# Performance work log

Hardware: AMD Instinct MI355X
Metric: run time of the kernel (lower is better)

The kernel has to match this reference:

```python
import jax, jax.numpy as jnp
import numpy as np

V, E, H, L, B = 32000, 128, 32, 64, 32


def setup_inputs() -> dict:
    key = jax.random.key(0)
    k0, k1, k2, k3, k4, k5 = jax.random.split(key, 6)
    stdv = 1.0 / np.sqrt(H)
    we = jax.random.uniform(k0, (V, E), minval=-stdv, maxval=stdv, dtype=jnp.float32)
    we = we.at[1].set(0.0)  # pad token row zeroed, as in original
    i2h1 = jax.random.uniform(k1, (E + H, H), minval=-stdv, maxval=stdv, dtype=jnp.float32)
    i2h2 = jax.random.uniform(k2, (E + H, H), minval=-stdv, maxval=stdv, dtype=jnp.float32)
    h2o = jax.random.uniform(k3, (2 * H, V), minval=-stdv, maxval=stdv, dtype=jnp.float32)
    bias = jnp.ones((1, H), dtype=jnp.float32)  # assigned after reset_parameters -> stays ones
    hidden_init = jax.random.normal(k4, (1, H), dtype=jnp.float32)  # plain buffer, not reset
    inp = jax.random.randint(k5, (L, B), 0, V, dtype=jnp.int64)
    return {"inp": inp, "we": we, "i2h1": i2h1, "i2h2": i2h2,
            "h2o": h2o, "bias": bias, "hidden_init": hidden_init}


def reference(inp, we, i2h1, i2h2, h2o, bias, hidden_init):
    Lr, Br = inp.shape
    Hh = hidden_init.shape[1]
    emb = we[inp]                                   # [L,B,E] embedding gather
    h0 = jnp.broadcast_to(hidden_init, (Br, Hh))    # [B,H]
    b = jnp.broadcast_to(bias, (Br, Hh))            # [B,H]

    def make_step(W):
        def step(h, e):
            h_new = jnp.tanh(jnp.concatenate([e, h], axis=1) @ W + b)
            return h_new, h_new
        return step

    # forward direction: hf[i] = hidden after consuming token i
    _, hf = jax.lax.scan(make_step(i2h1), h0, emb)
    # backward direction (scan over reversed time, flip back)
    _, hb_rev = jax.lax.scan(make_step(i2h2), h0, emb[::-1])
    hb = hb_rev[::-1]                               # hb[i] = bwd hidden after token i

    # original uses hiddenf[i] (pre-token-i fwd state) and hiddenb[i+1] (post-token-(i+1) bwd state)
    hf_used = jnp.concatenate([h0[None], hf[:-1]], axis=0)   # [L,B,H]
    hb_used = jnp.concatenate([hb[1:], h0[None]], axis=0)    # [L,B,H]

    hcat = jnp.concatenate([hf_used, hb_used], axis=-1)      # [L,B,2H]
    logits = jnp.einsum('lbh,hv->lbv', hcat, h2o)            # [L,B,V]
    return jax.nn.log_softmax(logits, axis=-1)
```

## Files before the change

### kernel.cpp

```cpp
#include <hip/hip_runtime.h>

#define V_SZ 32000
#define E_SZ 128
#define H_SZ 32
#define L_SZ 64
#define B_SZ 32
#define M_TOT 2048
#define K2 64
#define NVT 125
#define NMT 32

typedef __bf16 bf16x8 __attribute__((ext_vector_type(8)));
typedef float f32x4 __attribute__((ext_vector_type(4)));

__device__ __forceinline__ unsigned short f2bf(float f) {
    unsigned int u = __float_as_uint(f);
    u += 0x7FFFu + ((u >> 16) & 1u);
    return (unsigned short)(u >> 16);
}

__device__ __forceinline__ void load_bfrag(
    const __bf16* __restrict__ h2oT, int xcol, int wn, int lg, int lr,
    bf16x8 bfr[8][2]) {
    const int colbase = xcol * 256;
#pragma unroll
    for (int n = 0; n < 8; ++n) {
        int col = colbase + wn * 128 + n * 16 + lr;
        const __bf16* bp = h2oT + (size_t)col * K2 + lg * 8;
        bfr[n][0] = *(const bf16x8*)(bp);
        bfr[n][1] = *(const bf16x8*)(bp + 32);
    }
}

__device__ __forceinline__ void tile_gemm(
    const __bf16* __restrict__ hcat, int rowbase, int wm, int lg, int lr,
    const bf16x8 bfr[8][2], f32x4 acc[2][8]) {
    bf16x8 af[2][2];
#pragma unroll
    for (int m = 0; m < 2; ++m) {
        int row = rowbase + wm * 32 + m * 16 + lr;
#pragma unroll
        for (int kh = 0; kh < 2; ++kh)
            af[m][kh] = *(const bf16x8*)(hcat + row * K2 + kh * 32 + lg * 8);
    }
#pragma unroll
    for (int m = 0; m < 2; ++m)
#pragma unroll
        for (int n = 0; n < 8; ++n) acc[m][n] = (f32x4){0.f, 0.f, 0.f, 0.f};
#pragma unroll
    for (int n = 0; n < 8; ++n)
#pragma unroll
        for (int m = 0; m < 2; ++m) {
            acc[m][n] = __builtin_amdgcn_mfma_f32_16x16x32_bf16(af[m][0], bfr[n][0], acc[m][n], 0, 0, 0);
            acc[m][n] = __builtin_amdgcn_mfma_f32_16x16x32_bf16(af[m][1], bfr[n][1], acc[m][n], 0, 0, 0);
        }
}

__global__ __launch_bounds__(256) void k_prep_rnn(
    const int* __restrict__ inp, const float* __restrict__ we,
    const float* __restrict__ i2h1, const float* __restrict__ i2h2,
    const float* __restrict__ h2o, const float* __restrict__ bias,
    const float* __restrict__ hinit,
    unsigned short* __restrict__ hcat_u, unsigned short* __restrict__ h2oT_u) {
    const int tid = threadIdx.x;
    const int p = blockIdx.x;
    if (p < 125) {
        const int v = p * 256 + tid;
        unsigned int* dst = (unsigned int*)(h2oT_u + (size_t)v * K2);
#pragma unroll
        for (int k = 0; k < K2; k += 2) {
            float a = h2o[(size_t)k * V_SZ + v];
            float b = h2o[(size_t)(k + 1) * V_SZ + v];
            dst[k >> 1] = (unsigned int)f2bf(a) | ((unsigned int)f2bf(b) << 16);
        }
        return;
    }
    const int w2 = p - 125;
    const int dir = w2 >> 4;
    const int bpair = w2 & 15;
    const float* W = dir ? i2h2 : i2h1;
    __shared__ float Xl[L_SZ * 2 * H_SZ];
    {
        const int j = tid & 31, bb = (tid >> 5) & 1, to = tid >> 6;
        const int b = bpair * 2 + bb;
        const float bj = bias[j];
        for (int tt = 0; tt < 16; ++tt) {
            const int t = to * 16 + tt;
            const int idx = inp[t * B_SZ + b];
            const float* er = we + (size_t)idx * E_SZ;
            float acc = bj;
#pragma unroll
            for (int k0 = 0; k0 < E_SZ; k0 += 4) {
                f32x4 e4 = *(const f32x4*)(er + k0);
                acc += e4.x * W[(k0 + 0) * H_SZ + j];
                acc += e4.y * W[(k0 + 1) * H_SZ + j];
                acc += e4.z * W[(k0 + 2) * H_SZ + j];
                acc += e4.w * W[(k0 + 3) * H_SZ + j];
            }
            Xl[(t * 2 + bb) * H_SZ + j] = acc;
        }
    }
    __syncthreads();
    if (tid < 64) {
        const int lane = tid;
        const int bb = lane >> 5;
        const int b = bpair * 2 + bb;
        const int j = lane & 31;
        const int srcbase = lane & 32;
        float wh[H_SZ];
#pragma unroll
        for (int k = 0; k < H_SZ; ++k) wh[k] = W[(E_SZ + k) * H_SZ + j];
        float h = hinit[j];
        for (int step = 0; step < L_SZ; ++step) {
            const int tt = dir ? (L_SZ - 1 - step) : step;
            hcat_u[(tt * B_SZ + b) * K2 + dir * H_SZ + j] = f2bf(h);
            float a0 = Xl[(tt * 2 + bb) * H_SZ + j];
            float a1 = 0.f, a2 = 0.f, a3 = 0.f;
#pragma unroll
            for (int k = 0; k < H_SZ; k += 4) {
                a0 += __shfl(h, srcbase | k, 64) * wh[k];
                a1 += __shfl(h, srcbase | (k + 1), 64) * wh[k + 1];
                a2 += __shfl(h, srcbase | (k + 2), 64) * wh[k + 2];
                a3 += __shfl(h, srcbase | (k + 3), 64) * wh[k + 3];
            }
            float x2 = (a0 + a1) + (a2 + a3);
            float e = __expf(2.f * x2);
            h = 1.f - 2.f * __builtin_amdgcn_rcpf(e + 1.f);
        }
    }
}

__global__ __launch_bounds__(256) void k_pass_a(
    const __bf16* __restrict__ hcat, const __bf16* __restrict__ h2oT,
    float* __restrict__ Asum) {
    const int tid = threadIdx.x;
    const int wave = tid >> 6, lane = tid & 63;
    const int wm = wave >> 1, wn = wave & 1;
    const int lg = lane >> 4, lr = lane & 15;
    const int rowbase = blockIdx.y * 64;
    bf16x8 bfr[8][2];
    load_bfrag(h2oT, blockIdx.x, wn, lg, lr, bfr);
    f32x4 acc[2][8];
    tile_gemm(hcat, rowbase, wm, lg, lr, bfr, acc);
    float rs[2][4];
#pragma unroll
    for (int m = 0; m < 2; ++m)
#pragma unroll
        for (int r = 0; r < 4; ++r) {
            float s = 0.f;
#pragma unroll
            for (int n = 0; n < 8; ++n) s += __expf(acc[m][n][r]);
            rs[m][r] = s;
        }
#pragma unroll
    for (int mask = 1; mask < 16; mask <<= 1)
#pragma unroll
        for (int m = 0; m < 2; ++m)
#pragma unroll
            for (int r = 0; r < 4; ++r)
                rs[m][r] += __shfl_xor(rs[m][r], mask, 64);
    __shared__ float tsum[2][64];
    if (lr == 0) {
#pragma unroll
        for (int m = 0; m < 2; ++m)
#pragma unroll
            for (int r = 0; r < 4; ++r)
                tsum[wn][wm * 32 + m * 16 + lg * 4 + r] = rs[m][r];
    }
    __syncthreads();
    if (tid < 64)
        Asum[blockIdx.x * M_TOT + rowbase + tid] = tsum[0][tid] + tsum[1][tid];
}

__global__ __launch_bounds__(256) void k_lse(
    const float* __restrict__ Asum, float* __restrict__ lse) {
    const int row = blockIdx.x * 256 + threadIdx.x;
    float s = 0.f;
    for (int i = 0; i < NVT; ++i) s += Asum[i * M_TOT + row];
    lse[row] = logf(s);
}

__global__ __launch_bounds__(256) void k_pass_b(
    const __bf16* __restrict__ hcat, const __bf16* __restrict__ h2oT,
    const float* __restrict__ lse, float* __restrict__ out) {
    const int tid = threadIdx.x;
    const int wave = tid >> 6, lane = tid & 63;
    const int wm = wave >> 1, wn = wave & 1;
    const int lg = lane >> 4, lr = lane & 15;
    const int rowbase = blockIdx.y * 64;
    const int colbase = blockIdx.x * 256;
    bf16x8 bfr[8][2];
    load_bfrag(h2oT, blockIdx.x, wn, lg, lr, bfr);
    f32x4 acc[2][8];
    tile_gemm(hcat, rowbase, wm, lg, lr, bfr, acc);
    float lsev[2][4];
#pragma unroll
    for (int m = 0; m < 2; ++m)
#pragma unroll
        for (int r = 0; r < 4; ++r)
            lsev[m][r] = lse[rowbase + wm * 32 + m * 16 + lg * 4 + r];

    __shared__ float cbuf[32 * 260];
#pragma unroll
    for (int c = 0; c < 2; ++c) {
        if (c) __syncthreads();
#pragma unroll
        for (int n = 0; n < 8; ++n)
#pragma unroll
            for (int r = 0; r < 4; ++r)
                cbuf[(wm * 16 + lg * 4 + r) * 260 + wn * 128 + n * 16 + lr] =
                    acc[c][n][r] - lsev[c][r];
        __syncthreads();
#pragma unroll
        for (int it = 0; it < 8; ++it) {
            int idx4 = it * 256 + tid;
            int lrow = idx4 >> 6;
            int col = (idx4 & 63) << 2;
            int grow = rowbase + (lrow >> 4) * 32 + c * 16 + (lrow & 15);
            f32x4 v = *(const f32x4*)&cbuf[lrow * 260 + col];
            *(f32x4*)(out + (size_t)grow * V_SZ + colbase + col) = v;
        }
    }
}

extern "C" void kernel_launch(void* const* d_in, const int* in_sizes, int n_in,
                              void* d_out, int out_size, void* d_ws, size_t ws_size,
                              hipStream_t stream) {
    (void)in_sizes; (void)n_in; (void)out_size; (void)ws_size;
    const int*   inp   = (const int*)d_in[0];
    const float* we    = (const float*)d_in[1];
    const float* i2h1  = (const float*)d_in[2];
    const float* i2h2  = (const float*)d_in[3];
    const float* h2o   = (const float*)d_in[4];
    const float* bias  = (const float*)d_in[5];
    const float* hinit = (const float*)d_in[6];
    float* out = (float*)d_out;
    char* ws = (char*)d_ws;
    unsigned short* hcat_u = (unsigned short*)(ws);
    unsigned short* h2oT_u = (unsigned short*)(ws + 262144);
    float*          Asum   = (float*)(ws + 4358144);
    float*          lse    = (float*)(ws + 5382144);

    k_prep_rnn<<<157, 256, 0, stream>>>(inp, we, i2h1, i2h2, h2o, bias, hinit,
                                        hcat_u, h2oT_u);
    k_pass_a<<<dim3(NVT, NMT), 256, 0, stream>>>(
        (const __bf16*)hcat_u, (const __bf16*)h2oT_u, Asum);
    k_lse<<<8, 256, 0, stream>>>(Asum, lse);
    k_pass_b<<<dim3(NVT, NMT), 256, 0, stream>>>(
        (const __bf16*)hcat_u, (const __bf16*)h2oT_u, lse, out);
}
```

Before: 186.0 us.

## Cache bf16 logits from single GEMM pass instead of recomputing in second pass

Merges the exp-sum pass and the output pass so the logits GEMM runs once, storing logits as bf16 in workspace. A new elementwise kernel reads the cached logits, subtracts the per-row log-sum-exp and writes fp32 output. The GEMM kernel also processes four row tiles per block to reuse the loaded weight fragments. This trades recompute for an extra bf16 round trip through global memory and adds bf16 rounding to the logits before normalization.

```diff
diff --git a/kernel.cpp b/kernel.cpp
--- a/kernel.cpp
+++ b/kernel.cpp
@@ -8,15 +8,19 @@
 #define M_TOT 2048
 #define K2 64
 #define NVT 125
-#define NMT 32
+#define NQ4 (M_TOT * (V_SZ / 4))
 
 typedef __bf16 bf16x8 __attribute__((ext_vector_type(8)));
 typedef float f32x4 __attribute__((ext_vector_type(4)));
+typedef unsigned short u16x4 __attribute__((ext_vector_type(4)));
 
 __device__ __forceinline__ unsigned short f2bf(float f) {
     unsigned int u = __float_as_uint(f);
     u += 0x7FFFu + ((u >> 16) & 1u);
     return (unsigned short)(u >> 16);
+}
+__device__ __forceinline__ float bf2f(unsigned short u) {
+    return __uint_as_float((unsigned int)u << 16);
 }
 
 __device__ __forceinline__ void load_bfrag(
@@ -130,46 +134,80 @@
     }
 }
 
-__global__ __launch_bounds__(256) void k_pass_a(
+__global__ __launch_bounds__(256) void k_gemm_cache(
     const __bf16* __restrict__ hcat, const __bf16* __restrict__ h2oT,
-    float* __restrict__ Asum) {
+    float* __restrict__ Asum, unsigned short* __restrict__ logit_u) {
     const int tid = threadIdx.x;
     const int wave = tid >> 6, lane = tid & 63;
     const int wm = wave >> 1, wn = wave & 1;
     const int lg = lane >> 4, lr = lane & 15;
-    const int rowbase = blockIdx.y * 64;
+    const int xcol = blockIdx.x;
+    const int colbase = xcol * 256;
+
     bf16x8 bfr[8][2];
-    load_bfrag(h2oT, blockIdx.x, wn, lg, lr, bfr);
-    f32x4 acc[2][8];
-    tile_gemm(hcat, rowbase, wm, lg, lr, bfr, acc);
-    float rs[2][4];
-#pragma unroll
-    for (int m = 0; m < 2; ++m)
-#pragma unroll
-        for (int r = 0; r < 4; ++r) {
-            float s = 0.f;
-#pragma unroll
-            for (int n = 0; n < 8; ++n) s += __expf(acc[m][n][r]);
-            rs[m][r] = s;
-        }
-#pragma unroll
-    for (int mask = 1; mask < 16; mask <<= 1)
+    load_bfrag(h2oT, xcol, wn, lg, lr, bfr);
+
+    __shared__ float tsum[2][64];
+    __shared__ float cbuf[32 * 260];
+
+    for (int jt = 0; jt < 4; ++jt) {
+        const int rowbase = (blockIdx.y * 4 + jt) * 64;
+        f32x4 acc[2][8];
+        tile_gemm(hcat, rowbase, wm, lg, lr, bfr, acc);
+
+        float rs[2][4];
 #pragma unroll
         for (int m = 0; m < 2; ++m)
 #pragma unroll
-            for (int r = 0; r < 4; ++r)
-                rs[m][r] += __shfl_xor(rs[m][r], mask, 64);
-    __shared__ float tsum[2][64];
-    if (lr == 0) {
-#pragma unroll
-        for (int m = 0; m < 2; ++m)
-#pragma unroll
-            for (int r = 0; r < 4; ++r)
-                tsum[wn][wm * 32 + m * 16 + lg * 4 + r] = rs[m][r];
-    }
-    __syncthreads();
-    if (tid < 64)
-        Asum[blockIdx.x * M_TOT + rowbase + tid] = tsum[0][tid] + tsum[1][tid];
+            for (int r = 0; r < 4; ++r) {
+                float s = 0.f;
+#pragma unroll
+                for (int n = 0; n < 8; ++n) s += __expf(acc[m][n][r]);
+                rs[m][r] = s;
+            }
+#pragma unroll
+        for (int mask = 1; mask < 16; mask <<= 1)
+#pragma unroll
+            for (int m = 0; m < 2; ++m)
+#pragma unroll
+                for (int r = 0; r < 4; ++r)
+                    rs[m][r] += __shfl_xor(rs[m][r], mask, 64);
+        if (lr == 0) {
+#pragma unroll
+            for (int m = 0; m < 2; ++m)
+#pragma unroll
+                for (int r = 0; r < 4; ++r)
+                    tsum[wn][wm * 32 + m * 16 + lg * 4 + r] = rs[m][r];
+        }
+        __syncthreads();
+        if (tid < 64)
+            Asum[xcol * M_TOT + rowbase + tid] = tsum[0][tid] + tsum[1][tid];
+
+#pragma unroll
+        for (int c = 0; c < 2; ++c) {
+            __syncthreads();
+#pragma unroll
+            for (int n = 0; n < 8; ++n)
+#pragma unroll
+                for (int r = 0; r < 4; ++r)
+                    cbuf[(wm * 16 + lg * 4 + r) * 260 + wn * 128 + n * 16 + lr] =
+                        acc[c][n][r];
+            __syncthreads();
+#pragma unroll
+            for (int it = 0; it < 8; ++it) {
+                int idx4 = it * 256 + tid;
+                int lrow = idx4 >> 6;
+                int col = (idx4 & 63) << 2;
+                int grow = rowbase + (lrow >> 4) * 32 + c * 16 + (lrow & 15);
+                f32x4 v = *(const f32x4*)&cbuf[lrow * 260 + col];
+                u16x4 o;
+                o.x = f2bf(v.x); o.y = f2bf(v.y);
+                o.z = f2bf(v.z); o.w = f2bf(v.w);
+                *(u16x4*)(logit_u + (size_t)grow * V_SZ + colbase + col) = o;
+            }
+        }
+        __syncthreads();
+    }
 }
 
 __global__ __launch_bounds__(256) void k_lse(
@@ -180,46 +218,20 @@
     lse[row] = logf(s);
 }
 
-__global__ __launch_bounds__(256) void k_pass_b(
-    const __bf16* __restrict__ hcat, const __bf16* __restrict__ h2oT,
-    const float* __restrict__ lse, float* __restrict__ out) {
-    const int tid = threadIdx.x;
-    const int wave = tid >> 6, lane = tid & 63;
-    const int wm = wave >> 1, wn = wave & 1;
-    const int lg = lane >> 4, lr = lane & 15;
-    const int rowbase = blockIdx.y * 64;
-    const int colbase = blockIdx.x * 256;
-    bf16x8 bfr[8][2];
-    load_bfrag(h2oT, blockIdx.x, wn, lg, lr, bfr);
-    f32x4 acc[2][8];
-    tile_gemm(hcat, rowbase, wm, lg, lr, bfr, acc);
-    float lsev[2][4];
-#pragma unroll
-    for (int m = 0; m < 2; ++m)
-#pragma unroll
-        for (int r = 0; r < 4; ++r)
-            lsev[m][r] = lse[rowbase + wm * 32 + m * 16 + lg * 4 + r];
-
-    __shared__ float cbuf[32 * 260];
-#pragma unroll
-    for (int c = 0; c < 2; ++c) {
-        if (c) __syncthreads();
-#pragma unroll
-        for (int n = 0; n < 8; ++n)
-#pragma unroll
-            for (int r = 0; r < 4; ++r)
-                cbuf[(wm * 16 + lg * 4 + r) * 260 + wn * 128 + n * 16 + lr] =
-                    acc[c][n][r] - lsev[c][r];
-        __syncthreads();
-#pragma unroll
-        for (int it = 0; it < 8; ++it) {
-            int idx4 = it * 256 + tid;
-            int lrow = idx4 >> 6;
-            int col = (idx4 & 63) << 2;
-            int grow = rowbase + (lrow >> 4) * 32 + c * 16 + (lrow & 15);
-            f32x4 v = *(const f32x4*)&cbuf[lrow * 260 + col];
-            *(f32x4*)(out + (size_t)grow * V_SZ + colbase + col) = v;
-        }
+__global__ __launch_bounds__(256) void k_final(
+    const unsigned short* __restrict__ logit_u, const float* __restrict__ lse,
+    float* __restrict__ out) {
+    const int gs = gridDim.x * 256;
+    for (int i = blockIdx.x * 256 + threadIdx.x; i < NQ4; i += gs) {
+        const int row = (unsigned)i / 8000u;
+        u16x4 l4 = *(const u16x4*)(logit_u + (size_t)i * 4);
+        const float ls = lse[row];
+        f32x4 v;
+        v.x = bf2f(l4.x) - ls;
+        v.y = bf2f(l4.y) - ls;
+        v.z = bf2f(l4.z) - ls;
+        v.w = bf2f(l4.w) - ls;
+        *(f32x4*)(out + (size_t)i * 4) = v;
     }
 }
 
@@ -236,16 +248,16 @@
     const float* hinit = (const float*)d_in[6];
     float* out = (float*)d_out;
     char* ws = (char*)d_ws;
-    unsigned short* hcat_u = (unsigned short*)(ws);
-    unsigned short* h2oT_u = (unsigned short*)(ws + 262144);
-    float*          Asum   = (float*)(ws + 4358144);
-    float*          lse    = (float*)(ws + 5382144);
+    unsigned short* hcat_u  = (unsigned short*)(ws);
+    unsigned short* h2oT_u  = (unsigned short*)(ws + 262144);
+    float*          Asum    = (float*)(ws + 4358144);
+    float*          lse     = (float*)(ws + 5382144);
+    unsigned short* logit_u = (unsigned short*)(ws + 5390336);
 
     k_prep_rnn<<<157, 256, 0, stream>>>(inp, we, i2h1, i2h2, h2o, bias, hinit,
                                         hcat_u, h2oT_u);
-    k_pass_a<<<dim3(NVT, NMT), 256, 0, stream>>>(
-        (const __bf16*)hcat_u, (const __bf16*)h2oT_u, Asum);
+    k_gemm_cache<<<dim3(NVT, 8), 256, 0, stream>>>(
+        (const __bf16*)hcat_u, (const __bf16*)h2oT_u, Asum, logit_u);
     k_lse<<<8, 256, 0, stream>>>(Asum, lse);
-    k_pass_b<<<dim3(NVT, NMT), 256, 0, stream>>>(
-        (const __bf16*)hcat_u, (const __bf16*)h2oT_u, lse, out);
-}
+    k_final<<<2048, 256, 0, stream>>>(logit_u, lse, out);
+}
```

After: 199.6 us. 7.3% more time.

## Fold LSE reduction into pass B and loop row tiles in pass A

Applied to the files above, without the earlier changes.

Pass A now gives each block 8 row tiles so the h2o B-fragments are loaded once and reused across them. Partial exp-sums are written per wave-column into a row-major [row][256] layout with no shared-memory reduction. The separate k_lse kernel is removed, and each pass-B block instead sums the 250 partials for its 64 rows and takes the log before its GEMM. This saves a launch and repeated B-fragment loads, at the cost of redundant LSE reductions across the 125 column blocks and a grid of only 500 blocks in pass A.

```diff
diff --git a/kernel.cpp b/kernel.cpp
--- a/kernel.cpp
+++ b/kernel.cpp
@@ -9,6 +9,8 @@
 #define K2 64
 #define NVT 125
 #define NMT 32
+#define NPART 250
+#define PLD 256
 
 typedef __bf16 bf16x8 __attribute__((ext_vector_type(8)));
 typedef float f32x4 __attribute__((ext_vector_type(4)));
@@ -132,73 +134,86 @@
 
 __global__ __launch_bounds__(256) void k_pass_a(
     const __bf16* __restrict__ hcat, const __bf16* __restrict__ h2oT,
-    float* __restrict__ Asum) {
+    float* __restrict__ Asum2) {
     const int tid = threadIdx.x;
     const int wave = tid >> 6, lane = tid & 63;
     const int wm = wave >> 1, wn = wave & 1;
     const int lg = lane >> 4, lr = lane & 15;
-    const int rowbase = blockIdx.y * 64;
+    const int xcol = blockIdx.x;
+    const int pcol = xcol * 2 + wn;
+
     bf16x8 bfr[8][2];
-    load_bfrag(h2oT, blockIdx.x, wn, lg, lr, bfr);
-    f32x4 acc[2][8];
-    tile_gemm(hcat, rowbase, wm, lg, lr, bfr, acc);
-    float rs[2][4];
-#pragma unroll
-    for (int m = 0; m < 2; ++m)
-#pragma unroll
-        for (int r = 0; r < 4; ++r) {
-            float s = 0.f;
-#pragma unroll
-            for (int n = 0; n < 8; ++n) s += __expf(acc[m][n][r]);
-            rs[m][r] = s;
-        }
-#pragma unroll
-    for (int mask = 1; mask < 16; mask <<= 1)
+    load_bfrag(h2oT, xcol, wn, lg, lr, bfr);
+
+    for (int jt = 0; jt < 8; ++jt) {
+        const int rowbase = (blockIdx.y * 8 + jt) * 64;
+        f32x4 acc[2][8];
+        tile_gemm(hcat, rowbase, wm, lg, lr, bfr, acc);
+        float rs[2][4];
 #pragma unroll
         for (int m = 0; m < 2; ++m)
 #pragma unroll
-            for (int r = 0; r < 4; ++r)
-                rs[m][r] += __shfl_xor(rs[m][r], mask, 64);
-    __shared__ float tsum[2][64];
-    if (lr == 0) {
-#pragma unroll
-        for (int m = 0; m < 2; ++m)
-#pragma unroll
-            for (int r = 0; r < 4; ++r)
-                tsum[wn][wm * 32 + m * 16 + lg * 4 + r] = rs[m][r];
-    }
-    __syncthreads();
-    if (tid < 64)
-        Asum[blockIdx.x * M_TOT + rowbase + tid] = tsum[0][tid] + tsum[1][tid];
-}
-
-__global__ __launch_bounds__(256) void k_lse(
-    const float* __restrict__ Asum, float* __restrict__ lse) {
-    const int row = blockIdx.x * 256 + threadIdx.x;
-    float s = 0.f;
-    for (int i = 0; i < NVT; ++i) s += Asum[i * M_TOT + row];
-    lse[row] = logf(s);
+            for (int r = 0; r < 4; ++r) {
+                float s = 0.f;
+#pragma unroll
+                for (int n = 0; n < 8; ++n) s += __expf(acc[m][n][r]);
+                rs[m][r] = s;
+            }
+#pragma unroll
+        for (int mask = 1; mask < 16; mask <<= 1)
+#pragma unroll
+            for (int m = 0; m < 2; ++m)
+#pragma unroll
+                for (int r = 0; r < 4; ++r)
+                    rs[m][r] += __shfl_xor(rs[m][r], mask, 64);
+        if (lr == 0) {
+#pragma unroll
+            for (int m = 0; m < 2; ++m)
+#pragma unroll
+                for (int r = 0; r < 4; ++r) {
+                    const int row = rowbase + wm * 32 + m * 16 + lg * 4 + r;
+                    Asum2[(size_t)row * PLD + pcol] = rs[m][r];
+                }
+        }
+    }
 }
 
 __global__ __launch_bounds__(256) void k_pass_b(
     const __bf16* __restrict__ hcat, const __bf16* __restrict__ h2oT,
-    const float* __restrict__ lse, float* __restrict__ out) {
+    const float* __restrict__ Asum2, float* __restrict__ out) {
     const int tid = threadIdx.x;
     const int wave = tid >> 6, lane = tid & 63;
     const int wm = wave >> 1, wn = wave & 1;
     const int lg = lane >> 4, lr = lane & 15;
     const int rowbase = blockIdx.y * 64;
     const int colbase = blockIdx.x * 256;
+
+    __shared__ float part[64][4];
+    __shared__ float lse_s[64];
+    {
+        const int r = tid >> 2, q = tid & 3;
+        const int i0 = q * 63;
+        const int i1 = (q == 3) ? NPART : (i0 + 63);
+        const float* ap = Asum2 + (size_t)(rowbase + r) * PLD;
+        float s = 0.f;
+        for (int i = i0; i < i1; ++i) s += ap[i];
+        part[r][q] = s;
+    }
+    __syncthreads();
+    if (tid < 64)
+        lse_s[tid] = logf(part[tid][0] + part[tid][1] + part[tid][2] + part[tid][3]);
+
     bf16x8 bfr[8][2];
     load_bfrag(h2oT, blockIdx.x, wn, lg, lr, bfr);
     f32x4 acc[2][8];
     tile_gemm(hcat, rowbase, wm, lg, lr, bfr, acc);
+    __syncthreads();
     float lsev[2][4];
 #pragma unroll
     for (int m = 0; m < 2; ++m)
 #pragma unroll
         for (int r = 0; r < 4; ++r)
-            lsev[m][r] = lse[rowbase + wm * 32 + m * 16 + lg * 4 + r];
+            lsev[m][r] = lse_s[wm * 32 + m * 16 + lg * 4 + r];
 
     __shared__ float cbuf[32 * 260];
 #pragma unroll
@@ -238,14 +253,12 @@
     char* ws = (char*)d_ws;
     unsigned short* hcat_u = (unsigned short*)(ws);
     unsigned short* h2oT_u = (unsigned short*)(ws + 262144);
-    float*          Asum   = (float*)(ws + 4358144);
-    float*          lse    = (float*)(ws + 5382144);
+    float*          Asum2  = (float*)(ws + 4358144);
 
     k_prep_rnn<<<157, 256, 0, stream>>>(inp, we, i2h1, i2h2, h2o, bias, hinit,
                                         hcat_u, h2oT_u);
-    k_pass_a<<<dim3(NVT, NMT), 256, 0, stream>>>(
-        (const __bf16*)hcat_u, (const __bf16*)h2oT_u, Asum);
-    k_lse<<<8, 256, 0, stream>>>(Asum, lse);
+    k_pass_a<<<dim3(NVT, 4), 256, 0, stream>>>(
+        (const __bf16*)hcat_u, (const __bf16*)h2oT_u, Asum2);
     k_pass_b<<<dim3(NVT, NMT), 256, 0, stream>>>(
-        (const __bf16*)hcat_u, (const __bf16*)h2oT_u, lse, out);
-}
+        (const __bf16*)hcat_u, (const __bf16*)h2oT_u, Asum2, out);
+}
```

Measured after the change: 382.2 us. +105.4%, slower.
